# Performance work log

Measured on AMD Instinct MI355X. Metric: run time of the kernel, lower is better.

## Reference

```python
import jax, jax.numpy as jnp
import numpy as np

E = 128  # embedding_dim
C = 32   # per-head dim
H = 4    # heads
L = 256  # seq_len
N = 1    # batch


def layer_norm(x, gamma, beta, eps=1e-5):
    mu = jnp.mean(x, axis=-1, keepdims=True)
    var = jnp.mean((x - mu) ** 2, axis=-1, keepdims=True)
    return (x - mu) * jax.lax.rsqrt(var + eps) * gamma + beta


def setup_inputs() -> dict:
    key = jax.random.key(0)
    ks = jax.random.split(key, 12)
    s = E ** -0.5
    return {
        "pair_rep": jax.random.normal(ks[0], (N, L, L, E), dtype=jnp.float32),
        "mask": jax.random.normal(ks[1], (N, L, L), dtype=jnp.float32) * 0.1,
        "gamma": jnp.ones((E,), dtype=jnp.float32),
        "beta": jnp.zeros((E,), dtype=jnp.float32),
        "Wq": jax.random.normal(ks[2], (E, C * H), dtype=jnp.float32) * s,
        "Wk": jax.random.normal(ks[3], (E, C * H), dtype=jnp.float32) * s,
        "Wv": jax.random.normal(ks[4], (E, C * H), dtype=jnp.float32) * s,
        "Wb": jax.random.normal(ks[5], (E, H), dtype=jnp.float32) * s,
        "Wfu": jax.random.normal(ks[6], (E, C * H), dtype=jnp.float32) * s,
        "bfu": jnp.zeros((C * H,), dtype=jnp.float32),
        "Wo": jax.random.normal(ks[7], (C * H, E), dtype=jnp.float32) * (C * H) ** -0.5,
        "bo": jnp.zeros((E,), dtype=jnp.float32),
    }


def reference(pair_rep, mask, gamma, beta, Wq, Wk, Wv, Wb, Wfu, bfu, Wo, bo):
    n, s, _, _ = pair_rep.shape
    x = layer_norm(pair_rep, gamma, beta)  # [n,s,s,E]
    q = (x @ Wq).reshape(n, s, s, H, C) * (C ** -0.5)
    k = (x @ Wk).reshape(n, s, s, H, C)
    v = (x @ Wv).reshape(n, s, s, H, C)
    # faithful to original einsum: keys carry the q index, queries the v index
    dpa = jnp.einsum('nsqhc,nsvhc->nsqvh', k, q)  # [n,s,q,v,h]
    dpa = dpa + mask[:, None, :, :, None]
    pair_bias = x @ Wb  # [n,s,s,H]
    attn = jax.nn.softmax(dpa + pair_bias[:, None], axis=3)
    out = jnp.einsum('nsqvh,nsvhc->nsqhc', attn, v)  # [n,s,q,h,c]
    fu = jax.nn.sigmoid(x @ Wfu + bfu).reshape(n, s, s, H, C)
    out = out * fu
    out = out.reshape(n, s, s, H * C) @ Wo + bo
    return out
```

## Files before the change

kernel.cpp:

```cpp
#include <hip/hip_runtime.h>
#include <math.h>

#define L 256
#define E 128
#define H 4
#define C 32
#define P (L*L)

typedef __bf16 bf16;
typedef __bf16 bf16x8 __attribute__((ext_vector_type(8)));
typedef __bf16 bf16x4 __attribute__((ext_vector_type(4)));
typedef float  f32x4  __attribute__((ext_vector_type(4)));

#define MFMA(a,b,c) __builtin_amdgcn_mfma_f32_16x16x32_bf16((a),(b),(c),0,0,0)

__global__ __launch_bounds__(256) void k_prep(
    const float* __restrict__ Wq, const float* __restrict__ Wk,
    const float* __restrict__ Wv, const float* __restrict__ Wfu,
    const float* __restrict__ Wo, const float* __restrict__ Wb,
    bf16* __restrict__ WF, bf16* __restrict__ WoF, bf16* __restrict__ WbF)
{
  const int m = blockIdx.x;
  const int lane = threadIdx.x & 63, wv = threadIdx.x >> 6;
  const int g = lane >> 4, l15 = lane & 15;
  if (m < 5) {
    const float* W = (m==0)?Wq:(m==1)?Wk:(m==2)?Wv:(m==3)?Wfu:Wo;
    bf16* dst = (m < 4) ? (WF + (size_t)m * 16384) : WoF;
    const float sc = (m == 0) ? 0.17677669529663689f : 1.0f;
    for (int f = wv; f < 32; f += 4) {
      const int mt = f >> 2, kt = f & 3;
      const int row = 16*mt + l15, k0 = 32*kt + 8*g;
      bf16x8 o;
      #pragma unroll
      for (int j = 0; j < 8; ++j) o[j] = (bf16)(W[(size_t)(k0+j)*128 + row] * sc);
      *(bf16x8*)(dst + ((size_t)f*64 + lane)*8) = o;
    }
  } else {
    const int kt = wv, k0 = 32*kt + 8*g;
    bf16x8 o;
    #pragma unroll
    for (int j = 0; j < 8; ++j)
      o[j] = (l15 < 4) ? (bf16)Wb[(size_t)(k0+j)*4 + l15] : (bf16)0.0f;
    *(bf16x8*)(WbF + ((size_t)kt*64 + lane)*8) = o;
  }
}

__global__ __launch_bounds__(256) void k_ln_proj(
    const float* __restrict__ pr, const float* __restrict__ gamma,
    const float* __restrict__ beta, const float* __restrict__ bfu,
    const bf16* __restrict__ WF, const bf16* __restrict__ WbF,
    bf16* __restrict__ qbh, bf16* __restrict__ kbh, bf16* __restrict__ vbh,
    bf16* __restrict__ gfb, float* __restrict__ pbo)
{
  __shared__ bf16 xs[64 * 136];
  __shared__ bf16 stag[4][16 * 136];
  const int tid = threadIdx.x;
  const int base = blockIdx.x * 64;

  {
    const int pl = tid >> 2, sub = tid & 3;
    const float4* src = (const float4*)(pr + (size_t)(base + pl) * 128 + sub * 32);
    float4 r[8];
    float s = 0.f, ss = 0.f;
    #pragma unroll
    for (int j = 0; j < 8; ++j) {
      r[j] = src[j];
      s  += r[j].x + r[j].y + r[j].z + r[j].w;
      ss += r[j].x*r[j].x + r[j].y*r[j].y + r[j].z*r[j].z + r[j].w*r[j].w;
    }
    s  += __shfl_xor(s, 1, 4);  s  += __shfl_xor(s, 2, 4);
    ss += __shfl_xor(ss, 1, 4); ss += __shfl_xor(ss, 2, 4);
    const float mu   = s * 0.0078125f;
    const float var  = ss * 0.0078125f - mu * mu;
    const float rstd = rsqrtf(var + 1e-5f);
    const float4* g4 = (const float4*)(gamma + sub * 32);
    const float4* b4 = (const float4*)(beta + sub * 32);
    bf16* xr = xs + pl * 136 + sub * 32;
    #pragma unroll
    for (int i = 0; i < 4; ++i) {
      float4 r0 = r[2*i], r1 = r[2*i+1];
      float4 gg0 = g4[2*i], gg1 = g4[2*i+1], bb0 = b4[2*i], bb1 = b4[2*i+1];
      bf16x8 o;
      o[0] = (bf16)((r0.x - mu) * rstd * gg0.x + bb0.x);
      o[1] = (bf16)((r0.y - mu) * rstd * gg0.y + bb0.y);
      o[2] = (bf16)((r0.z - mu) * rstd * gg0.z + bb0.z);
      o[3] = (bf16)((r0.w - mu) * rstd * gg0.w + bb0.w);
      o[4] = (bf16)((r1.x - mu) * rstd * gg1.x + bb1.x);
      o[5] = (bf16)((r1.y - mu) * rstd * gg1.y + bb1.y);
      o[6] = (bf16)((r1.z - mu) * rstd * gg1.z + bb1.z);
      o[7] = (bf16)((r1.w - mu) * rstd * gg1.w + bb1.w);
      *(bf16x8*)(xr + 8 * i) = o;
    }
  }
  __syncthreads();

  const int w = tid >> 6, lane = tid & 63, g = lane >> 4, l15 = lane & 15;
  const f32x4 z = {0.f, 0.f, 0.f, 0.f};

  {
    f32x4 acc = z;
    #pragma unroll
    for (int kt = 0; kt < 4; ++kt) {
      bf16x8 a = *(const bf16x8*)(WbF + ((size_t)kt*64 + lane)*8);
      bf16x8 b = *(const bf16x8*)(xs + (16*w + l15)*136 + 32*kt + 8*g);
      acc = MFMA(a, b, acc);
    }
    if (g == 0)
      *(float4*)(pbo + (size_t)(base + 16*w + l15)*4) =
          make_float4(acc[0], acc[1], acc[2], acc[3]);
  }

  const bf16* WFw = WF + (size_t)w * 16384;
  bf16* stw = stag[w];

  for (int nt = 0; nt < 4; ++nt) {
    bf16x8 bfr[4];
    #pragma unroll
    for (int kt = 0; kt < 4; ++kt)
      bfr[kt] = *(const bf16x8*)(xs + (16*nt + l15)*136 + 32*kt + 8*g);
    f32x4 acc[8];
    #pragma unroll
    for (int mt = 0; mt < 8; ++mt) acc[mt] = z;
    #pragma unroll
    for (int kt = 0; kt < 4; ++kt)
      #pragma unroll
      for (int mt = 0; mt < 8; ++mt) {
        bf16x8 a = *(const bf16x8*)(WFw + ((size_t)(mt*4 + kt)*64 + lane)*8);
        acc[mt] = MFMA(a, bfr[kt], acc[mt]);
      }

    #pragma unroll
    for (int mt = 0; mt < 8; ++mt) {
      const int col = 16*mt + 4*g;
      f32x4 vv = acc[mt];
      if (w == 3) {
        float4 bb = *(const float4*)(bfu + col);
        vv[0] = 1.f / (1.f + __expf(-(vv[0] + bb.x)));
        vv[1] = 1.f / (1.f + __expf(-(vv[1] + bb.y)));
        vv[2] = 1.f / (1.f + __expf(-(vv[2] + bb.z)));
        vv[3] = 1.f / (1.f + __expf(-(vv[3] + bb.w)));
      }
      bf16x4 o;
      o[0] = (bf16)vv[0]; o[1] = (bf16)vv[1]; o[2] = (bf16)vv[2]; o[3] = (bf16)vv[3];
      *(bf16x4*)(stw + l15*136 + col) = o;
    }

    #pragma unroll
    for (int i = 0; i < 4; ++i) {
      const int flat = i*512 + lane*8;
      const int p = flat >> 7, c = flat & 127;
      bf16x8 val = *(const bf16x8*)(stw + p*136 + c);
      if (w == 3) {
        *(bf16x8*)(gfb + ((size_t)(base + 16*nt + p))*128 + c) = val;
      } else {
        bf16* dst = (w == 0) ? qbh : (w == 1) ? kbh : vbh;
        const int h = c >> 5;
        *(bf16x8*)(dst + ((size_t)h*P + base + 16*nt + p)*32 + (c & 31)) = val;
      }
    }
  }
}

__global__ __launch_bounds__(256) void k_bias(
    const float* __restrict__ mask, const float* __restrict__ pb,
    bf16* __restrict__ T4)
{
  const int b = blockIdx.x, h = b >> 4, qt = b & 15;
  const int v = threadIdx.x;
  bf16 row[16];
  #pragma unroll
  for (int q16 = 0; q16 < 16; ++q16) {
    const int q = qt*16 + q16;
    row[q16] = (bf16)(mask[(size_t)q*256 + v] + pb[((size_t)q*256 + v)*4 + h]);
  }
  bf16* dst = T4 + ((size_t)b*256 + v)*16;
  *(bf16x8*)(dst)     = *(bf16x8*)(row);
  *(bf16x8*)(dst + 8) = *(bf16x8*)(row + 8);
}

__global__ __launch_bounds__(256) void k_attn(
    const bf16* __restrict__ qbh, const bf16* __restrict__ kbh,
    const bf16* __restrict__ vbh, const bf16* __restrict__ T4,
    bf16* __restrict__ aob)
{
  __shared__ bf16 qs[256 * 40];
  __shared__ bf16 ps[4][16 * 264];
  const int tid = threadIdx.x;
  const int s = blockIdx.x >> 2, h = blockIdx.x & 3;
  const int rb = s * 256;
  const bf16* qh = qbh + (size_t)h * P * 32;
  const bf16* kh = kbh + (size_t)h * P * 32;
  const bf16* vh = vbh + (size_t)h * P * 32;
  bf16* vT = &ps[0][0];

  #pragma unroll
  for (int i = 0; i < 4; ++i) {
    const int flat = i*2048 + tid*8;
    const int pos = flat >> 5, cc = flat & 31;
    bf16x8 qv = *(const bf16x8*)(qh + ((size_t)rb + pos)*32 + cc);
    *(bf16x8*)(qs + pos*40 + cc) = qv;
    bf16x8 vv = *(const bf16x8*)(vh + ((size_t)rb + pos)*32 + cc);
    #pragma unroll
    for (int j = 0; j < 8; ++j) vT[(cc + j)*264 + pos] = vv[j];
  }
  __syncthreads();

  const int w = tid >> 6, lane = tid & 63, g = lane >> 4, l15 = lane & 15;

  bf16x8 av[2][8];
  #pragma unroll
  for (int mt = 0; mt < 2; ++mt)
    #pragma unroll
    for (int kt = 0; kt < 8; ++kt)
      av[mt][kt] = *(const bf16x8*)(vT + (16*mt + l15)*264 + 32*kt + 8*g);
  __syncthreads();

  bf16* psw = ps[w];
  const bf16* T4h = T4 + (size_t)h * 16 * 4096;
  bf16* aoh = aob + (size_t)h * P * 32;
  const f32x4 z = {0.f, 0.f, 0.f, 0.f};

  for (int qt = 0; qt < 4; ++qt) {
    const int q0 = w*64 + qt*16;

    const bf16* Tsl = T4h + (size_t)(q0 >> 4) * 4096;
    #pragma unroll
    for (int i = 0; i < 8; ++i) {
      const int flat = i*512 + lane*8;
      *(bf16x8*)(psw + flat) = *(const bf16x8*)(Tsl + flat);
    }

    bf16x8 ak = *(const bf16x8*)(kh + ((size_t)rb + q0 + l15)*32 + 8*g);
    f32x4 sc[16];
    #pragma unroll
    for (int t = 0; t < 16; ++t) {
      bf16x8 bq = *(const bf16x8*)(qs + (16*t + l15)*40 + 8*g);
      sc[t] = MFMA(ak, bq, z);
    }

    float rs0 = 0.f, rs1 = 0.f, rs2 = 0.f, rs3 = 0.f;
    #pragma unroll
    for (int t = 0; t < 16; ++t) {
      bf16x4 bb = *(const bf16x4*)(psw + (16*t + l15)*16 + 4*g);
      float e0 = __expf(sc[t][0] + (float)bb[0]); sc[t][0] = e0; rs0 += e0;
      float e1 = __expf(sc[t][1] + (float)bb[1]); sc[t][1] = e1; rs1 += e1;
      float e2 = __expf(sc[t][2] + (float)bb[2]); sc[t][2] = e2; rs2 += e2;
      float e3 = __expf(sc[t][3] + (float)bb[3]); sc[t][3] = e3; rs3 += e3;
    }
    #pragma unroll
    for (int m = 1; m < 16; m <<= 1) {
      rs0 += __shfl_xor(rs0, m, 16);
      rs1 += __shfl_xor(rs1, m, 16);
      rs2 += __shfl_xor(rs2, m, 16);
      rs3 += __shfl_xor(rs3, m, 16);
    }
    const float i0 = 1.f/rs0, i1 = 1.f/rs1, i2 = 1.f/rs2, i3 = 1.f/rs3;

    #pragma unroll
    for (int t = 0; t < 16; ++t) {
      const int vcol = 16*t + l15;
      psw[(4*g + 0)*264 + vcol] = (bf16)(sc[t][0] * i0);
      psw[(4*g + 1)*264 + vcol] = (bf16)(sc[t][1] * i1);
      psw[(4*g + 2)*264 + vcol] = (bf16)(sc[t][2] * i2);
      psw[(4*g + 3)*264 + vcol] = (bf16)(sc[t][3] * i3);
    }

    f32x4 o0 = z, o1 = z;
    #pragma unroll
    for (int kt = 0; kt < 8; ++kt) {
      bf16x8 bp = *(const bf16x8*)(psw + l15*264 + 32*kt + 8*g);
      o0 = MFMA(av[0][kt], bp, o0);
      o1 = MFMA(av[1][kt], bp, o1);
    }
    bf16x4 p0, p1;
    p0[0] = (bf16)o0[0]; p0[1] = (bf16)o0[1]; p0[2] = (bf16)o0[2]; p0[3] = (bf16)o0[3];
    p1[0] = (bf16)o1[0]; p1[1] = (bf16)o1[1]; p1[2] = (bf16)o1[2]; p1[3] = (bf16)o1[3];
    bf16* dst = aoh + ((size_t)rb + q0 + l15)*32;
    *(bf16x4*)(dst + 4*g)      = p0;
    *(bf16x4*)(dst + 16 + 4*g) = p1;
  }
}

__global__ __launch_bounds__(256) void k_gate_out(
    const bf16* __restrict__ aob, const bf16* __restrict__ gfb,
    const bf16* __restrict__ WoF, const float* __restrict__ bo,
    float* __restrict__ out)
{
  __shared__ bf16 gs[64 * 136];
  const int tid = threadIdx.x;
  const int base = blockIdx.x * 64;

  #pragma unroll
  for (int i = 0; i < 4; ++i) {
    const int flat = i*2048 + tid*8;
    const int pos = flat >> 7, c = flat & 127, h = c >> 5;
    bf16x8 a = *(const bf16x8*)(aob + ((size_t)h*P + base + pos)*32 + (c & 31));
    bf16x8 f = *(const bf16x8*)(gfb + ((size_t)(base + pos))*128 + c);
    bf16x8 o;
    #pragma unroll
    for (int j = 0; j < 8; ++j) o[j] = (bf16)((float)a[j] * (float)f[j]);
    *(bf16x8*)(gs + pos*136 + c) = o;
  }
  __syncthreads();

  const int w = tid >> 6, lane = tid & 63, g = lane >> 4, l15 = lane & 15;
  const f32x4 z = {0.f, 0.f, 0.f, 0.f};

  for (int nt = 0; nt < 4; ++nt) {
    bf16x8 bfr[4];
    #pragma unroll
    for (int kt = 0; kt < 4; ++kt)
      bfr[kt] = *(const bf16x8*)(gs + (16*nt + l15)*136 + 32*kt + 8*g);
    f32x4 a0 = z, a1 = z;
    #pragma unroll
    for (int kt = 0; kt < 4; ++kt) {
      bf16x8 af0 = *(const bf16x8*)(WoF + ((size_t)((2*w+0)*4 + kt)*64 + lane)*8);
      bf16x8 af1 = *(const bf16x8*)(WoF + ((size_t)((2*w+1)*4 + kt)*64 + lane)*8);
      a0 = MFMA(af0, bfr[kt], a0);
      a1 = MFMA(af1, bfr[kt], a1);
    }
    const int pos = base + 16*nt + l15;
    {
      const int col = 16*(2*w + 0) + 4*g;
      float4 bb = *(const float4*)(bo + col);
      *(float4*)(out + (size_t)pos*128 + col) =
          make_float4(a0[0] + bb.x, a0[1] + bb.y, a0[2] + bb.z, a0[3] + bb.w);
    }
    {
      const int col = 16*(2*w + 1) + 4*g;
      float4 bb = *(const float4*)(bo + col);
      *(float4*)(out + (size_t)pos*128 + col) =
          make_float4(a1[0] + bb.x, a1[1] + bb.y, a1[2] + bb.z, a1[3] + bb.w);
    }
  }
}

extern "C" void kernel_launch(void* const* d_in, const int* in_sizes, int n_in,
                              void* d_out, int out_size, void* d_ws, size_t ws_size,
                              hipStream_t stream) {
  const float* pr    = (const float*)d_in[0];
  const float* mask  = (const float*)d_in[1];
  const float* gamma = (const float*)d_in[2];
  const float* beta  = (const float*)d_in[3];
  const float* Wq    = (const float*)d_in[4];
  const float* Wk    = (const float*)d_in[5];
  const float* Wv    = (const float*)d_in[6];
  const float* Wb    = (const float*)d_in[7];
  const float* Wfu   = (const float*)d_in[8];
  const float* bfu   = (const float*)d_in[9];
  const float* Wo    = (const float*)d_in[10];
  const float* bo    = (const float*)d_in[11];
  float* out = (float*)d_out;

  bf16* qbh = (bf16*)d_ws;
  bf16* kbh = qbh + (size_t)H * P * 32;
  bf16* vbh = kbh + (size_t)H * P * 32;
  bf16* gfb = vbh + (size_t)H * P * 32;
  bf16* aob = gfb + (size_t)P * 128;
  bf16* T4  = aob + (size_t)H * P * 32;
  bf16* WF  = T4  + (size_t)H * P;
  bf16* WoF = WF  + 4 * 16384;
  bf16* WbF = WoF + 16384;
  float* pb = (float*)(WbF + 2048);

  k_prep<<<6, 256, 0, stream>>>(Wq, Wk, Wv, Wfu, Wo, Wb, WF, WoF, WbF);
  k_ln_proj<<<1024, 256, 0, stream>>>(pr, gamma, beta, bfu, WF, WbF,
                                      qbh, kbh, vbh, gfb, pb);
  k_bias<<<64, 256, 0, stream>>>(mask, pb, T4);
  k_attn<<<1024, 256, 0, stream>>>(qbh, kbh, vbh, T4, aob);
  k_gate_out<<<1024, 256, 0, stream>>>(aob, gfb, WoF, bo, out);
}
```

Before: 200.1 us.

## Pre-swizzle V and bias into MFMA fragment layouts, swap attention operand roles

The projection kernel now writes V directly in MFMA A-fragment order and stores the pair bias head-major, so the attention kernel no longer stages Q and transposed V through shared memory. Attention keeps Q fragments in registers as the A operand with K as B, which turns the per-row softmax reduction into two cross-lane shuffles instead of four 16-lane reductions. The bias tensor is emitted in the exact per-lane fragment order with coalesced float4 reads. The projection processes two 16-row tiles per pass to reuse weight fragments, and Wo fragments are hoisted out of the output-GEMM loop. The cost is extra register pressure and a scattered LDS gather for the V swizzle.

New measurement: 214.8 us. 1.07x slower.

```diff
diff --git a/kernel.cpp b/kernel.cpp
--- a/kernel.cpp
+++ b/kernel.cpp
@@ -49,13 +49,14 @@
     const float* __restrict__ pr, const float* __restrict__ gamma,
     const float* __restrict__ beta, const float* __restrict__ bfu,
     const bf16* __restrict__ WF, const bf16* __restrict__ WbF,
-    bf16* __restrict__ qbh, bf16* __restrict__ kbh, bf16* __restrict__ vbh,
+    bf16* __restrict__ qbh, bf16* __restrict__ kbh, bf16* __restrict__ vF,
     bf16* __restrict__ gfb, float* __restrict__ pbo)
 {
   __shared__ bf16 xs[64 * 136];
-  __shared__ bf16 stag[4][16 * 136];
+  __shared__ bf16 stag[4][32 * 132];
   const int tid = threadIdx.x;
   const int base = blockIdx.x * 64;
+  const int sblk = blockIdx.x >> 2;
 
   {
     const int pl = tid >> 2, sub = tid & 3;
@@ -105,172 +106,170 @@
       bf16x8 b = *(const bf16x8*)(xs + (16*w + l15)*136 + 32*kt + 8*g);
       acc = MFMA(a, b, acc);
     }
-    if (g == 0)
-      *(float4*)(pbo + (size_t)(base + 16*w + l15)*4) =
-          make_float4(acc[0], acc[1], acc[2], acc[3]);
+    if (g == 0) {
+      #pragma unroll
+      for (int r = 0; r < 4; ++r)
+        pbo[(size_t)r*P + base + 16*w + l15] = acc[r];
+    }
   }
 
   const bf16* WFw = WF + (size_t)w * 16384;
   bf16* stw = stag[w];
 
-  for (int nt = 0; nt < 4; ++nt) {
-    bf16x8 bfr[4];
-    #pragma unroll
-    for (int kt = 0; kt < 4; ++kt)
-      bfr[kt] = *(const bf16x8*)(xs + (16*nt + l15)*136 + 32*kt + 8*g);
-    f32x4 acc[8];
-    #pragma unroll
-    for (int mt = 0; mt < 8; ++mt) acc[mt] = z;
+  for (int ntp = 0; ntp < 2; ++ntp) {
+    bf16x8 bfr[2][4];
+    #pragma unroll
+    for (int p = 0; p < 2; ++p)
+      #pragma unroll
+      for (int kt = 0; kt < 4; ++kt)
+        bfr[p][kt] = *(const bf16x8*)(xs + (32*ntp + 16*p + l15)*136 + 32*kt + 8*g);
+
+    f32x4 acc[8][2];
+    #pragma unroll
+    for (int mt = 0; mt < 8; ++mt) { acc[mt][0] = z; acc[mt][1] = z; }
     #pragma unroll
     for (int kt = 0; kt < 4; ++kt)
       #pragma unroll
       for (int mt = 0; mt < 8; ++mt) {
         bf16x8 a = *(const bf16x8*)(WFw + ((size_t)(mt*4 + kt)*64 + lane)*8);
-        acc[mt] = MFMA(a, bfr[kt], acc[mt]);
+        acc[mt][0] = MFMA(a, bfr[0][kt], acc[mt][0]);
+        acc[mt][1] = MFMA(a, bfr[1][kt], acc[mt][1]);
       }
 
     #pragma unroll
     for (int mt = 0; mt < 8; ++mt) {
       const int col = 16*mt + 4*g;
-      f32x4 vv = acc[mt];
-      if (w == 3) {
-        float4 bb = *(const float4*)(bfu + col);
-        vv[0] = 1.f / (1.f + __expf(-(vv[0] + bb.x)));
-        vv[1] = 1.f / (1.f + __expf(-(vv[1] + bb.y)));
-        vv[2] = 1.f / (1.f + __expf(-(vv[2] + bb.z)));
-        vv[3] = 1.f / (1.f + __expf(-(vv[3] + bb.w)));
+      #pragma unroll
+      for (int p = 0; p < 2; ++p) {
+        f32x4 vv = acc[mt][p];
+        if (w == 3) {
+          float4 bb = *(const float4*)(bfu + col);
+          vv[0] = 1.f / (1.f + __expf(-(vv[0] + bb.x)));
+          vv[1] = 1.f / (1.f + __expf(-(vv[1] + bb.y)));
+          vv[2] = 1.f / (1.f + __expf(-(vv[2] + bb.z)));
+          vv[3] = 1.f / (1.f + __expf(-(vv[3] + bb.w)));
+        }
+        bf16x4 o;
+        o[0] = (bf16)vv[0]; o[1] = (bf16)vv[1]; o[2] = (bf16)vv[2]; o[3] = (bf16)vv[3];
+        *(bf16x4*)(stw + (16*p + l15)*132 + col) = o;
       }
-      bf16x4 o;
-      o[0] = (bf16)vv[0]; o[1] = (bf16)vv[1]; o[2] = (bf16)vv[2]; o[3] = (bf16)vv[3];
-      *(bf16x4*)(stw + l15*136 + col) = o;
-    }
-
-    #pragma unroll
-    for (int i = 0; i < 4; ++i) {
-      const int flat = i*512 + lane*8;
-      const int p = flat >> 7, c = flat & 127;
-      bf16x8 val = *(const bf16x8*)(stw + p*136 + c);
-      if (w == 3) {
-        *(bf16x8*)(gfb + ((size_t)(base + 16*nt + p))*128 + c) = val;
-      } else {
-        bf16* dst = (w == 0) ? qbh : (w == 1) ? kbh : vbh;
-        const int h = c >> 5;
-        *(bf16x8*)(dst + ((size_t)h*P + base + 16*nt + p)*32 + (c & 31)) = val;
+    }
+
+    if (w == 2) {
+      const int ktg = (blockIdx.x & 3)*2 + ntp;
+      #pragma unroll
+      for (int h = 0; h < 4; ++h)
+        #pragma unroll
+        for (int mt2 = 0; mt2 < 2; ++mt2) {
+          bf16x8 o;
+          #pragma unroll
+          for (int j = 0; j < 8; ++j)
+            o[j] = stw[(8*(lane >> 4) + j)*132 + h*32 + 16*mt2 + (lane & 15)];
+          *(bf16x8*)(vF + (((size_t)(h*256 + sblk)*16 + mt2*8 + ktg)*64 + lane)*8) = o;
+        }
+    } else {
+      #pragma unroll
+      for (int i = 0; i < 8; ++i) {
+        const int flat = i*512 + lane*8;
+        const int p2 = flat >> 7, c = flat & 127;
+        bf16x8 val = *(const bf16x8*)(stw + p2*132 + c);
+        if (w == 3) {
+          *(bf16x8*)(gfb + ((size_t)(base + 32*ntp + p2))*128 + c) = val;
+        } else {
+          bf16* dst = (w == 0) ? qbh : kbh;
+          const int h2 = c >> 5;
+          *(bf16x8*)(dst + ((size_t)h2*P + base + 32*ntp + p2)*32 + (c & 31)) = val;
+        }
       }
     }
   }
 }
 
-__global__ __launch_bounds__(256) void k_bias(
+__global__ __launch_bounds__(256) void k_bias6(
     const float* __restrict__ mask, const float* __restrict__ pb,
-    bf16* __restrict__ T4)
-{
-  const int b = blockIdx.x, h = b >> 4, qt = b & 15;
-  const int v = threadIdx.x;
-  bf16 row[16];
+    bf16* __restrict__ T6)
+{
+  const int b = blockIdx.x, h = b >> 4;
+  const int lane = threadIdx.x & 63, tg = threadIdx.x >> 6;
+  const int g = lane >> 4, l15 = lane & 15;
+  const int q = (b & 15)*16 + l15;
+  const float* mrow = mask + (size_t)q * 256;
+  const float* prow = pb + (size_t)h * P + (size_t)q * 256;
   #pragma unroll
-  for (int q16 = 0; q16 < 16; ++q16) {
-    const int q = qt*16 + q16;
-    row[q16] = (bf16)(mask[(size_t)q*256 + v] + pb[((size_t)q*256 + v)*4 + h]);
-  }
-  bf16* dst = T4 + ((size_t)b*256 + v)*16;
-  *(bf16x8*)(dst)     = *(bf16x8*)(row);
-  *(bf16x8*)(dst + 8) = *(bf16x8*)(row + 8);
+  for (int tt = 0; tt < 4; ++tt) {
+    const int t = tg*4 + tt, v0 = 16*t + 4*g;
+    float4 m4 = *(const float4*)(mrow + v0);
+    float4 p4 = *(const float4*)(prow + v0);
+    bf16x4 o;
+    o[0] = (bf16)(m4.x + p4.x); o[1] = (bf16)(m4.y + p4.y);
+    o[2] = (bf16)(m4.z + p4.z); o[3] = (bf16)(m4.w + p4.w);
+    *(bf16x4*)(T6 + (((size_t)b*16 + t)*64 + lane)*4) = o;
+  }
 }
 
 __global__ __launch_bounds__(256) void k_attn(
     const bf16* __restrict__ qbh, const bf16* __restrict__ kbh,
-    const bf16* __restrict__ vbh, const bf16* __restrict__ T4,
+    const bf16* __restrict__ vF, const bf16* __restrict__ T6,
     bf16* __restrict__ aob)
 {
-  __shared__ bf16 qs[256 * 40];
   __shared__ bf16 ps[4][16 * 264];
   const int tid = threadIdx.x;
   const int s = blockIdx.x >> 2, h = blockIdx.x & 3;
   const int rb = s * 256;
+  const int w = tid >> 6, lane = tid & 63, g = lane >> 4, l15 = lane & 15;
   const bf16* qh = qbh + (size_t)h * P * 32;
   const bf16* kh = kbh + (size_t)h * P * 32;
-  const bf16* vh = vbh + (size_t)h * P * 32;
-  bf16* vT = &ps[0][0];
-
-  #pragma unroll
-  for (int i = 0; i < 4; ++i) {
-    const int flat = i*2048 + tid*8;
-    const int pos = flat >> 5, cc = flat & 31;
-    bf16x8 qv = *(const bf16x8*)(qh + ((size_t)rb + pos)*32 + cc);
-    *(bf16x8*)(qs + pos*40 + cc) = qv;
-    bf16x8 vv = *(const bf16x8*)(vh + ((size_t)rb + pos)*32 + cc);
-    #pragma unroll
-    for (int j = 0; j < 8; ++j) vT[(cc + j)*264 + pos] = vv[j];
-  }
-  __syncthreads();
-
-  const int w = tid >> 6, lane = tid & 63, g = lane >> 4, l15 = lane & 15;
-
-  bf16x8 av[2][8];
-  #pragma unroll
-  for (int mt = 0; mt < 2; ++mt)
-    #pragma unroll
-    for (int kt = 0; kt < 8; ++kt)
-      av[mt][kt] = *(const bf16x8*)(vT + (16*mt + l15)*264 + 32*kt + 8*g);
-  __syncthreads();
-
+  const bf16* vFh = vF + ((size_t)(h*256 + s)*16)*512;
   bf16* psw = ps[w];
-  const bf16* T4h = T4 + (size_t)h * 16 * 4096;
   bf16* aoh = aob + (size_t)h * P * 32;
   const f32x4 z = {0.f, 0.f, 0.f, 0.f};
 
+  bf16x8 aq[16];
+  #pragma unroll
+  for (int t = 0; t < 16; ++t)
+    aq[t] = *(const bf16x8*)(qh + ((size_t)rb + 16*t + l15)*32 + 8*g);
+
   for (int qt = 0; qt < 4; ++qt) {
     const int q0 = w*64 + qt*16;
 
-    const bf16* Tsl = T4h + (size_t)(q0 >> 4) * 4096;
-    #pragma unroll
-    for (int i = 0; i < 8; ++i) {
-      const int flat = i*512 + lane*8;
-      *(bf16x8*)(psw + flat) = *(const bf16x8*)(Tsl + flat);
-    }
-
-    bf16x8 ak = *(const bf16x8*)(kh + ((size_t)rb + q0 + l15)*32 + 8*g);
+    bf16x8 bk = *(const bf16x8*)(kh + ((size_t)rb + q0 + l15)*32 + 8*g);
+
     f32x4 sc[16];
     #pragma unroll
+    for (int t = 0; t < 16; ++t) sc[t] = MFMA(aq[t], bk, z);
+
+    const bf16* Tq = T6 + ((size_t)(h*16 + w*4 + qt)*16)*256;
+    float rs = 0.f;
+    #pragma unroll
     for (int t = 0; t < 16; ++t) {
-      bf16x8 bq = *(const bf16x8*)(qs + (16*t + l15)*40 + 8*g);
-      sc[t] = MFMA(ak, bq, z);
-    }
-
-    float rs0 = 0.f, rs1 = 0.f, rs2 = 0.f, rs3 = 0.f;
+      bf16x4 bb = *(const bf16x4*)(Tq + ((size_t)t*64 + lane)*4);
+      float e0 = __expf(sc[t][0] + (float)bb[0]);
+      float e1 = __expf(sc[t][1] + (float)bb[1]);
+      float e2 = __expf(sc[t][2] + (float)bb[2]);
+      float e3 = __expf(sc[t][3] + (float)bb[3]);
+      sc[t][0] = e0; sc[t][1] = e1; sc[t][2] = e2; sc[t][3] = e3;
+      rs += (e0 + e1) + (e2 + e3);
+    }
+    rs += __shfl_xor(rs, 16);
+    rs += __shfl_xor(rs, 32);
+    const float inv = 1.f / rs;
+
     #pragma unroll
     for (int t = 0; t < 16; ++t) {
-      bf16x4 bb = *(const bf16x4*)(psw + (16*t + l15)*16 + 4*g);
-      float e0 = __expf(sc[t][0] + (float)bb[0]); sc[t][0] = e0; rs0 += e0;
-      float e1 = __expf(sc[t][1] + (float)bb[1]); sc[t][1] = e1; rs1 += e1;
-      float e2 = __expf(sc[t][2] + (float)bb[2]); sc[t][2] = e2; rs2 += e2;
-      float e3 = __expf(sc[t][3] + (float)bb[3]); sc[t][3] = e3; rs3 += e3;
-    }
-    #pragma unroll
-    for (int m = 1; m < 16; m <<= 1) {
-      rs0 += __shfl_xor(rs0, m, 16);
-      rs1 += __shfl_xor(rs1, m, 16);
-      rs2 += __shfl_xor(rs2, m, 16);
-      rs3 += __shfl_xor(rs3, m, 16);
-    }
-    const float i0 = 1.f/rs0, i1 = 1.f/rs1, i2 = 1.f/rs2, i3 = 1.f/rs3;
-
-    #pragma unroll
-    for (int t = 0; t < 16; ++t) {
-      const int vcol = 16*t + l15;
-      psw[(4*g + 0)*264 + vcol] = (bf16)(sc[t][0] * i0);
-      psw[(4*g + 1)*264 + vcol] = (bf16)(sc[t][1] * i1);
-      psw[(4*g + 2)*264 + vcol] = (bf16)(sc[t][2] * i2);
-      psw[(4*g + 3)*264 + vcol] = (bf16)(sc[t][3] * i3);
+      bf16x4 o;
+      o[0] = (bf16)(sc[t][0] * inv); o[1] = (bf16)(sc[t][1] * inv);
+      o[2] = (bf16)(sc[t][2] * inv); o[3] = (bf16)(sc[t][3] * inv);
+      *(bf16x4*)(psw + l15*264 + 16*t + 4*g) = o;
     }
 
     f32x4 o0 = z, o1 = z;
     #pragma unroll
     for (int kt = 0; kt < 8; ++kt) {
       bf16x8 bp = *(const bf16x8*)(psw + l15*264 + 32*kt + 8*g);
-      o0 = MFMA(av[0][kt], bp, o0);
-      o1 = MFMA(av[1][kt], bp, o1);
+      bf16x8 a0 = *(const bf16x8*)(vFh + ((size_t)(kt)*64 + lane)*8);
+      bf16x8 a1 = *(const bf16x8*)(vFh + ((size_t)(8 + kt)*64 + lane)*8);
+      o0 = MFMA(a0, bp, o0);
+      o1 = MFMA(a1, bp, o1);
     }
     bf16x4 p0, p1;
     p0[0] = (bf16)o0[0]; p0[1] = (bf16)o0[1]; p0[2] = (bf16)o0[2]; p0[3] = (bf16)o0[3];
@@ -306,6 +305,13 @@
   const int w = tid >> 6, lane = tid & 63, g = lane >> 4, l15 = lane & 15;
   const f32x4 z = {0.f, 0.f, 0.f, 0.f};
 
+  bf16x8 af[2][4];
+  #pragma unroll
+  for (int mi = 0; mi < 2; ++mi)
+    #pragma unroll
+    for (int kt = 0; kt < 4; ++kt)
+      af[mi][kt] = *(const bf16x8*)(WoF + ((size_t)((2*w + mi)*4 + kt)*64 + lane)*8);
+
   for (int nt = 0; nt < 4; ++nt) {
     bf16x8 bfr[4];
     #pragma unroll
@@ -314,10 +320,8 @@
     f32x4 a0 = z, a1 = z;
     #pragma unroll
     for (int kt = 0; kt < 4; ++kt) {
-      bf16x8 af0 = *(const bf16x8*)(WoF + ((size_t)((2*w+0)*4 + kt)*64 + lane)*8);
-      bf16x8 af1 = *(const bf16x8*)(WoF + ((size_t)((2*w+1)*4 + kt)*64 + lane)*8);
-      a0 = MFMA(af0, bfr[kt], a0);
-      a1 = MFMA(af1, bfr[kt], a1);
+      a0 = MFMA(af[0][kt], bfr[kt], a0);
+      a1 = MFMA(af[1][kt], bfr[kt], a1);
     }
     const int pos = base + 16*nt + l15;
     {
@@ -354,19 +358,19 @@
 
   bf16* qbh = (bf16*)d_ws;
   bf16* kbh = qbh + (size_t)H * P * 32;
-  bf16* vbh = kbh + (size_t)H * P * 32;
-  bf16* gfb = vbh + (size_t)H * P * 32;
+  bf16* vF  = kbh + (size_t)H * P * 32;
+  bf16* gfb = vF  + (size_t)H * P * 32;
   bf16* aob = gfb + (size_t)P * 128;
-  bf16* T4  = aob + (size_t)H * P * 32;
-  bf16* WF  = T4  + (size_t)H * P;
+  bf16* T6  = aob + (size_t)H * P * 32;
+  bf16* WF  = T6  + (size_t)H * P;
   bf16* WoF = WF  + 4 * 16384;
   bf16* WbF = WoF + 16384;
   float* pb = (float*)(WbF + 2048);
 
   k_prep<<<6, 256, 0, stream>>>(Wq, Wk, Wv, Wfu, Wo, Wb, WF, WoF, WbF);
   k_ln_proj<<<1024, 256, 0, stream>>>(pr, gamma, beta, bfu, WF, WbF,
-                                      qbh, kbh, vbh, gfb, pb);
-  k_bias<<<64, 256, 0, stream>>>(mask, pb, T4);
-  k_attn<<<1024, 256, 0, stream>>>(qbh, kbh, vbh, T4, aob);
+                                      qbh, kbh, vF, gfb, pb);
+  k_bias6<<<64, 256, 0, stream>>>(mask, pb, T6);
+  k_attn<<<1024, 256, 0, stream>>>(qbh, kbh, vF, T6, aob);
   k_gate_out<<<1024, 256, 0, stream>>>(aob, gfb, WoF, bo, out);
 }
```
